# Performance work log

Hardware: AMD Instinct MI355X
Metric: run time of the kernel (lower is better)

Reference implementation:

```python
import jax, jax.numpy as jnp
from jax import lax
import numpy as np

N, D = 1024, 100000
K, SELECT_N = 20, 256  # select_n = int(N * split) = int(1024 * 0.25)


def setup_inputs() -> dict:
    key = jax.random.key(0)
    k1, k2 = jax.random.split(key)
    inp = jax.random.normal(k1, (N, D), dtype=jnp.float32)
    indices = jax.random.randint(k2, (K, SELECT_N), 0, N, dtype=jnp.int32)
    return {"inp": inp, "indices": indices}


def reference(inp, indices):
    # For each of k bagging rounds: gather select_n random rows, max over rows.
    # scan over k keeps the peak intermediate at [select_n, D] instead of [k, select_n, D].
    def step(_, idx):
        return None, jnp.max(inp[idx], axis=0)  # [D]

    _, maxes = lax.scan(step, None, indices)   # [k, D]
    return jnp.mean(maxes, axis=0, keepdims=True)  # [1, D]
```

## Files before the change

kernel.cpp:

```cpp
#include <hip/hip_runtime.h>


#define N_ROWS   1024
#define D_COLS   100000
#define K_ROUNDS 20
#define SEL_N    256
#define NIDX     (K_ROUNDS * SEL_N)
#define CPB      16
#define NBLOCKS  (D_COLS / CPB)
#define BLOCK    256
#define WAVES    4
#define RNDS_PW  (K_ROUNDS / WAVES)
#define NXCD     8
#define NEG_INF  (-3.402823466e+38f)

__global__ __launch_bounds__(BLOCK, 2) void bagmax_kernel(
    const float* __restrict__ inp,
    const int*   __restrict__ indices,
    float*       __restrict__ out)
{
    __shared__ float tile[N_ROWS * CPB];
    __shared__ __align__(16) unsigned short sidx[NIDX];
    __shared__ float wpart[WAVES][CPB];

    const int tid  = threadIdx.x;
    const int lane = tid & 63;
    const int wave = tid >> 6;

    const int orig = blockIdx.x;
    const int q    = NBLOCKS / NXCD;
    const int r8   = NBLOCKS % NXCD;
    const int xcd  = orig & (NXCD - 1);
    const int slot = orig >> 3;
    const int wg   = (xcd < r8 ? xcd * (q + 1) : r8 * (q + 1) + (xcd - r8) * q) + slot;
    const int colbase = wg * CPB;

    for (int i = tid; i < NIDX; i += BLOCK) {
        const int p   = i & 255;
        const int dst = (i & ~255) | ((p & 15) << 4) | (p >> 4);
        sidx[dst] = (unsigned short)indices[i];
    }

    {
        const int ro = tid >> 2;
        const int c4 = (tid & 3) * 4;
        const float* gp = inp + (size_t)ro * D_COLS + colbase + c4;
        #pragma unroll
        for (int it = 0; it < 16; ++it) {
            const int r = it * 64 + ro;
            const float4 v = *reinterpret_cast<const float4*>(gp + (size_t)it * 64 * D_COLS);
            *reinterpret_cast<float4*>(&tile[r * CPB + c4]) = v;
        }
    }
    __syncthreads();

    const int g = lane >> 2;
    const int u = lane & 3;

    float4 rsum = make_float4(0.f, 0.f, 0.f, 0.f);
    #pragma unroll
    for (int kk = 0; kk < RNDS_PW; ++kk) {
        const int k = wave * RNDS_PW + kk;

        const uint4* sp = reinterpret_cast<const uint4*>(&sidx[k * SEL_N + g * 16]);
        const uint4 w0 = sp[0];
        const uint4 w1 = sp[1];
        unsigned int e[16];
        e[0]  = w0.x & 0xFFFFu; e[1]  = w0.x >> 16;
        e[2]  = w0.y & 0xFFFFu; e[3]  = w0.y >> 16;
        e[4]  = w0.z & 0xFFFFu; e[5]  = w0.z >> 16;
        e[6]  = w0.w & 0xFFFFu; e[7]  = w0.w >> 16;
        e[8]  = w1.x & 0xFFFFu; e[9]  = w1.x >> 16;
        e[10] = w1.y & 0xFFFFu; e[11] = w1.y >> 16;
        e[12] = w1.z & 0xFFFFu; e[13] = w1.z >> 16;
        e[14] = w1.w & 0xFFFFu; e[15] = w1.w >> 16;

        float4 a0 = make_float4(NEG_INF, NEG_INF, NEG_INF, NEG_INF);
        float4 a1 = a0;
        #pragma unroll
        for (int i = 0; i < 16; i += 2) {
            const float4 v0 = *reinterpret_cast<const float4*>(&tile[e[i]     * CPB + u * 4]);
            const float4 v1 = *reinterpret_cast<const float4*>(&tile[e[i + 1] * CPB + u * 4]);
            a0.x = fmaxf(a0.x, v0.x); a0.y = fmaxf(a0.y, v0.y);
            a0.z = fmaxf(a0.z, v0.z); a0.w = fmaxf(a0.w, v0.w);
            a1.x = fmaxf(a1.x, v1.x); a1.y = fmaxf(a1.y, v1.y);
            a1.z = fmaxf(a1.z, v1.z); a1.w = fmaxf(a1.w, v1.w);
        }
        float4 acc;
        acc.x = fmaxf(a0.x, a1.x); acc.y = fmaxf(a0.y, a1.y);
        acc.z = fmaxf(a0.z, a1.z); acc.w = fmaxf(a0.w, a1.w);

        #pragma unroll
        for (int s = 4; s <= 32; s <<= 1) {
            acc.x = fmaxf(acc.x, __shfl_xor(acc.x, s, 64));
            acc.y = fmaxf(acc.y, __shfl_xor(acc.y, s, 64));
            acc.z = fmaxf(acc.z, __shfl_xor(acc.z, s, 64));
            acc.w = fmaxf(acc.w, __shfl_xor(acc.w, s, 64));
        }
        rsum.x += acc.x; rsum.y += acc.y; rsum.z += acc.z; rsum.w += acc.w;
    }

    if (g == 0) *reinterpret_cast<float4*>(&wpart[wave][u * 4]) = rsum;
    __syncthreads();

    if (tid < CPB) {
        const float s = wpart[0][tid] + wpart[1][tid] + wpart[2][tid] + wpart[3][tid];
        out[colbase + tid] = s * (1.0f / (float)K_ROUNDS);
    }
}

extern "C" void kernel_launch(void* const* d_in, const int* in_sizes, int n_in,
                              void* d_out, int out_size, void* d_ws, size_t ws_size,
                              hipStream_t stream) {
    const float* inp     = (const float*)d_in[0];
    const int*   indices = (const int*)d_in[1];
    float*       out     = (float*)d_out;

    bagmax_kernel<<<NBLOCKS, BLOCK, 0, stream>>>(inp, indices, out);
}
```

Before: 116.7 us.

## Use persistent blocks with producer/consumer waves and double-buffered LDS tiles

Replaces the one-block-per-16-column-tile launch with a persistent grid of 256 blocks of 512 threads. Four producer waves prefetch the next column tile from global memory into a second LDS buffer while four consumer waves compute the bagged max/mean on the current tile. This hides global load latency behind compute and avoids reloading the index table for every tile. The cost is one block per CU, a __syncthreads per tile, and a grid of only 256 blocks, which may leave CUs underused and reduce memory-level parallelism. The XCD-aware block remapping is also dropped.

```diff
diff --git a/kernel.cpp b/kernel.cpp
--- a/kernel.cpp
+++ b/kernel.cpp
@@ -7,33 +7,25 @@
 #define SEL_N    256
 #define NIDX     (K_ROUNDS * SEL_N)
 #define CPB      16
-#define NBLOCKS  (D_COLS / CPB)
-#define BLOCK    256
-#define WAVES    4
-#define RNDS_PW  (K_ROUNDS / WAVES)
-#define NXCD     8
+#define NT       (D_COLS / CPB)
+#define BLOCK    512
+#define GRID     256
+#define CWAVES   4
+#define RNDS_PW  (K_ROUNDS / CWAVES)
 #define NEG_INF  (-3.402823466e+38f)
 
-__global__ __launch_bounds__(BLOCK, 2) void bagmax_kernel(
+__global__ __launch_bounds__(BLOCK, 1) void bagmax_kernel(
     const float* __restrict__ inp,
     const int*   __restrict__ indices,
     float*       __restrict__ out)
 {
-    __shared__ float tile[N_ROWS * CPB];
+    __shared__ float tile[2][N_ROWS * CPB];
     __shared__ __align__(16) unsigned short sidx[NIDX];
-    __shared__ float wpart[WAVES][CPB];
+    __shared__ float wpart[2][CWAVES][CPB];
 
-    const int tid  = threadIdx.x;
-    const int lane = tid & 63;
-    const int wave = tid >> 6;
-
-    const int orig = blockIdx.x;
-    const int q    = NBLOCKS / NXCD;
-    const int r8   = NBLOCKS % NXCD;
-    const int xcd  = orig & (NXCD - 1);
-    const int slot = orig >> 3;
-    const int wg   = (xcd < r8 ? xcd * (q + 1) : r8 * (q + 1) + (xcd - r8) * q) + slot;
-    const int colbase = wg * CPB;
+    const int tid = threadIdx.x;
+    const int b   = blockIdx.x;
+    const int cnt = (NT - b + GRID - 1) / GRID;
 
     for (int i = tid; i < NIDX; i += BLOCK) {
         const int p   = i & 255;
@@ -42,70 +34,106 @@
     }
 
     {
+        const int colbase = b * CPB;
         const int ro = tid >> 2;
         const int c4 = (tid & 3) * 4;
         const float* gp = inp + (size_t)ro * D_COLS + colbase + c4;
         #pragma unroll
-        for (int it = 0; it < 16; ++it) {
-            const int r = it * 64 + ro;
-            const float4 v = *reinterpret_cast<const float4*>(gp + (size_t)it * 64 * D_COLS);
-            *reinterpret_cast<float4*>(&tile[r * CPB + c4]) = v;
+        for (int it = 0; it < 8; ++it) {
+            const int r = it * 128 + ro;
+            const float4 v = *reinterpret_cast<const float4*>(gp + (size_t)it * 128 * D_COLS);
+            *reinterpret_cast<float4*>(&tile[0][r * CPB + c4]) = v;
         }
     }
     __syncthreads();
 
-    const int g = lane >> 2;
-    const int u = lane & 3;
+    const bool prod = (tid >= 256);
+    const int lane  = tid & 63;
+    const int wave  = (tid >> 6) & 3;
+    const int g     = lane >> 2;
+    const int u     = lane & 3;
 
-    float4 rsum = make_float4(0.f, 0.f, 0.f, 0.f);
-    #pragma unroll
-    for (int kk = 0; kk < RNDS_PW; ++kk) {
-        const int k = wave * RNDS_PW + kk;
+    #pragma unroll 1
+    for (int i = 0; i < cnt; ++i) {
+        const int cur = i & 1;
 
-        const uint4* sp = reinterpret_cast<const uint4*>(&sidx[k * SEL_N + g * 16]);
-        const uint4 w0 = sp[0];
-        const uint4 w1 = sp[1];
-        unsigned int e[16];
-        e[0]  = w0.x & 0xFFFFu; e[1]  = w0.x >> 16;
-        e[2]  = w0.y & 0xFFFFu; e[3]  = w0.y >> 16;
-        e[4]  = w0.z & 0xFFFFu; e[5]  = w0.z >> 16;
-        e[6]  = w0.w & 0xFFFFu; e[7]  = w0.w >> 16;
-        e[8]  = w1.x & 0xFFFFu; e[9]  = w1.x >> 16;
-        e[10] = w1.y & 0xFFFFu; e[11] = w1.y >> 16;
-        e[12] = w1.z & 0xFFFFu; e[13] = w1.z >> 16;
-        e[14] = w1.w & 0xFFFFu; e[15] = w1.w >> 16;
+        if (prod) {
+            if (i + 1 < cnt) {
+                const int ncol = (b + (i + 1) * GRID) * CPB;
+                const int ptid = tid - 256;
+                const int ro = ptid >> 2;
+                const int c4 = (ptid & 3) * 4;
+                const float* gp = inp + (size_t)ro * D_COLS + ncol + c4;
+                float* tb = &tile[cur ^ 1][0];
+                #pragma unroll
+                for (int it = 0; it < 16; ++it) {
+                    const int r = it * 64 + ro;
+                    const float4 v = *reinterpret_cast<const float4*>(gp + (size_t)it * 64 * D_COLS);
+                    *reinterpret_cast<float4*>(&tb[r * CPB + c4]) = v;
+                }
+            }
+        } else {
+            if (i > 0 && tid < CPB) {
+                const int pcol = (b + (i - 1) * GRID) * CPB;
+                const float s = wpart[cur ^ 1][0][tid] + wpart[cur ^ 1][1][tid]
+                              + wpart[cur ^ 1][2][tid] + wpart[cur ^ 1][3][tid];
+                out[pcol + tid] = s * (1.0f / (float)K_ROUNDS);
+            }
 
-        float4 a0 = make_float4(NEG_INF, NEG_INF, NEG_INF, NEG_INF);
-        float4 a1 = a0;
-        #pragma unroll
-        for (int i = 0; i < 16; i += 2) {
-            const float4 v0 = *reinterpret_cast<const float4*>(&tile[e[i]     * CPB + u * 4]);
-            const float4 v1 = *reinterpret_cast<const float4*>(&tile[e[i + 1] * CPB + u * 4]);
-            a0.x = fmaxf(a0.x, v0.x); a0.y = fmaxf(a0.y, v0.y);
-            a0.z = fmaxf(a0.z, v0.z); a0.w = fmaxf(a0.w, v0.w);
-            a1.x = fmaxf(a1.x, v1.x); a1.y = fmaxf(a1.y, v1.y);
-            a1.z = fmaxf(a1.z, v1.z); a1.w = fmaxf(a1.w, v1.w);
+            const float* tb = &tile[cur][0];
+            float4 rsum = make_float4(0.f, 0.f, 0.f, 0.f);
+            #pragma unroll
+            for (int kk = 0; kk < RNDS_PW; ++kk) {
+                const int k = wave * RNDS_PW + kk;
+
+                const uint4* sp = reinterpret_cast<const uint4*>(&sidx[k * SEL_N + g * 16]);
+                const uint4 w0 = sp[0];
+                const uint4 w1 = sp[1];
+                unsigned int e[16];
+                e[0]  = w0.x & 0xFFFFu; e[1]  = w0.x >> 16;
+                e[2]  = w0.y & 0xFFFFu; e[3]  = w0.y >> 16;
+                e[4]  = w0.z & 0xFFFFu; e[5]  = w0.z >> 16;
+                e[6]  = w0.w & 0xFFFFu; e[7]  = w0.w >> 16;
+                e[8]  = w1.x & 0xFFFFu; e[9]  = w1.x >> 16;
+                e[10] = w1.y & 0xFFFFu; e[11] = w1.y >> 16;
+                e[12] = w1.z & 0xFFFFu; e[13] = w1.z >> 16;
+                e[14] = w1.w & 0xFFFFu; e[15] = w1.w >> 16;
+
+                float4 a0 = make_float4(NEG_INF, NEG_INF, NEG_INF, NEG_INF);
+                float4 a1 = a0;
+                #pragma unroll
+                for (int j = 0; j < 16; j += 2) {
+                    const float4 v0 = *reinterpret_cast<const float4*>(&tb[e[j]     * CPB + u * 4]);
+                    const float4 v1 = *reinterpret_cast<const float4*>(&tb[e[j + 1] * CPB + u * 4]);
+                    a0.x = fmaxf(a0.x, v0.x); a0.y = fmaxf(a0.y, v0.y);
+                    a0.z = fmaxf(a0.z, v0.z); a0.w = fmaxf(a0.w, v0.w);
+                    a1.x = fmaxf(a1.x, v1.x); a1.y = fmaxf(a1.y, v1.y);
+                    a1.z = fmaxf(a1.z, v1.z); a1.w = fmaxf(a1.w, v1.w);
+                }
+                float4 acc;
+                acc.x = fmaxf(a0.x, a1.x); acc.y = fmaxf(a0.y, a1.y);
+                acc.z = fmaxf(a0.z, a1.z); acc.w = fmaxf(a0.w, a1.w);
+
+                #pragma unroll
+                for (int s = 4; s <= 32; s <<= 1) {
+                    acc.x = fmaxf(acc.x, __shfl_xor(acc.x, s, 64));
+                    acc.y = fmaxf(acc.y, __shfl_xor(acc.y, s, 64));
+                    acc.z = fmaxf(acc.z, __shfl_xor(acc.z, s, 64));
+                    acc.w = fmaxf(acc.w, __shfl_xor(acc.w, s, 64));
+                }
+                rsum.x += acc.x; rsum.y += acc.y; rsum.z += acc.z; rsum.w += acc.w;
+            }
+            if (g == 0) *reinterpret_cast<float4*>(&wpart[cur][wave][u * 4]) = rsum;
         }
-        float4 acc;
-        acc.x = fmaxf(a0.x, a1.x); acc.y = fmaxf(a0.y, a1.y);
-        acc.z = fmaxf(a0.z, a1.z); acc.w = fmaxf(a0.w, a1.w);
-
-        #pragma unroll
-        for (int s = 4; s <= 32; s <<= 1) {
-            acc.x = fmaxf(acc.x, __shfl_xor(acc.x, s, 64));
-            acc.y = fmaxf(acc.y, __shfl_xor(acc.y, s, 64));
-            acc.z = fmaxf(acc.z, __shfl_xor(acc.z, s, 64));
-            acc.w = fmaxf(acc.w, __shfl_xor(acc.w, s, 64));
-        }
-        rsum.x += acc.x; rsum.y += acc.y; rsum.z += acc.z; rsum.w += acc.w;
+        __syncthreads();
     }
 
-    if (g == 0) *reinterpret_cast<float4*>(&wpart[wave][u * 4]) = rsum;
-    __syncthreads();
-
     if (tid < CPB) {
-        const float s = wpart[0][tid] + wpart[1][tid] + wpart[2][tid] + wpart[3][tid];
-        out[colbase + tid] = s * (1.0f / (float)K_ROUNDS);
+        const int pb   = (cnt - 1) & 1;
+        const int pcol = (b + (cnt - 1) * GRID) * CPB;
+        const float s = wpart[pb][0][tid] + wpart[pb][1][tid]
+                      + wpart[pb][2][tid] + wpart[pb][3][tid];
+        out[pcol + tid] = s * (1.0f / (float)K_ROUNDS);
     }
 }
 
@@ -116,5 +144,5 @@
     const int*   indices = (const int*)d_in[1];
     float*       out     = (float*)d_out;
 
-    bagmax_kernel<<<NBLOCKS, BLOCK, 0, stream>>>(inp, indices, out);
+    bagmax_kernel<<<GRID, BLOCK, 0, stream>>>(inp, indices, out);
 }
```

Measured after the change: 128.3 us. 1.1x slower.

## Use persistent grid with double-buffered LDS tile prefetch and DPP reductions

Applied to the files above, without the earlier changes.

Replaces the one-block-per-16-column launch with a persistent grid of 256 blocks. Each block loops over column tiles and prefetches the next tile into registers while reducing the current one from a double-buffered LDS tile. This amortizes the per-block index staging and launch cost and overlaps global loads with LDS gather work. Part of the cross-lane max reduction now uses DPP row shifts instead of shuffles. The trade-off is lower occupancy (launch bounds 1, doubled LDS, many prefetch registers) and fewer blocks to hide memory latency.

```diff
diff --git a/kernel.cpp b/kernel.cpp
--- a/kernel.cpp
+++ b/kernel.cpp
@@ -7,19 +7,28 @@
 #define SEL_N    256
 #define NIDX     (K_ROUNDS * SEL_N)
 #define CPB      16
-#define NBLOCKS  (D_COLS / CPB)
+#define NT       (D_COLS / CPB)
 #define BLOCK    256
+#define GRID     256
 #define WAVES    4
 #define RNDS_PW  (K_ROUNDS / WAVES)
-#define NXCD     8
 #define NEG_INF  (-3.402823466e+38f)
 
-__global__ __launch_bounds__(BLOCK, 2) void bagmax_kernel(
+template<int CTRL>
+__device__ __forceinline__ float dpp_shr_max(float x) {
+    const int xi = __float_as_int(x);
+    const int sh = __builtin_amdgcn_update_dpp(xi, xi, CTRL, 0xF, 0xF, false);
+    return fmaxf(x, __int_as_float(sh));
+}
+#define ROW_SHR4 0x114
+#define ROW_SHR8 0x118
+
+__global__ __launch_bounds__(BLOCK, 1) void bagmax_kernel(
     const float* __restrict__ inp,
     const int*   __restrict__ indices,
     float*       __restrict__ out)
 {
-    __shared__ float tile[N_ROWS * CPB];
+    __shared__ float tile[2][N_ROWS * CPB];
     __shared__ __align__(16) unsigned short sidx[NIDX];
     __shared__ float wpart[WAVES][CPB];
 
@@ -27,13 +36,9 @@
     const int lane = tid & 63;
     const int wave = tid >> 6;
 
-    const int orig = blockIdx.x;
-    const int q    = NBLOCKS / NXCD;
-    const int r8   = NBLOCKS % NXCD;
-    const int xcd  = orig & (NXCD - 1);
-    const int slot = orig >> 3;
-    const int wg   = (xcd < r8 ? xcd * (q + 1) : r8 * (q + 1) + (xcd - r8) * q) + slot;
-    const int colbase = wg * CPB;
+    const int b   = blockIdx.x;
+    const int swz = (b & 7) * 32 + (b >> 3);
+    const int cnt = (NT - swz + GRID - 1) / GRID;
 
     for (int i = tid; i < NIDX; i += BLOCK) {
         const int p   = i & 255;
@@ -41,71 +46,104 @@
         sidx[dst] = (unsigned short)indices[i];
     }
 
+    const int ro = tid >> 2;
+    const int c4 = (tid & 3) * 4;
+
     {
-        const int ro = tid >> 2;
-        const int c4 = (tid & 3) * 4;
-        const float* gp = inp + (size_t)ro * D_COLS + colbase + c4;
+        const float* gp = inp + (size_t)ro * D_COLS + swz * CPB + c4;
+        float4 v[16];
         #pragma unroll
-        for (int it = 0; it < 16; ++it) {
-            const int r = it * 64 + ro;
-            const float4 v = *reinterpret_cast<const float4*>(gp + (size_t)it * 64 * D_COLS);
-            *reinterpret_cast<float4*>(&tile[r * CPB + c4]) = v;
-        }
+        for (int it = 0; it < 16; ++it)
+            v[it] = *reinterpret_cast<const float4*>(gp + (size_t)it * 64 * D_COLS);
+        #pragma unroll
+        for (int it = 0; it < 16; ++it)
+            *reinterpret_cast<float4*>(&tile[0][(it * 64 + ro) * CPB + c4]) = v[it];
     }
     __syncthreads();
 
     const int g = lane >> 2;
     const int u = lane & 3;
 
-    float4 rsum = make_float4(0.f, 0.f, 0.f, 0.f);
-    #pragma unroll
-    for (int kk = 0; kk < RNDS_PW; ++kk) {
-        const int k = wave * RNDS_PW + kk;
+    #pragma unroll 1
+    for (int i = 0; i < cnt; ++i) {
+        const int cur = i & 1;
+        const bool havenext = (i + 1 < cnt);
 
-        const uint4* sp = reinterpret_cast<const uint4*>(&sidx[k * SEL_N + g * 16]);
-        const uint4 w0 = sp[0];
-        const uint4 w1 = sp[1];
-        unsigned int e[16];
-        e[0]  = w0.x & 0xFFFFu; e[1]  = w0.x >> 16;
-        e[2]  = w0.y & 0xFFFFu; e[3]  = w0.y >> 16;
-        e[4]  = w0.z & 0xFFFFu; e[5]  = w0.z >> 16;
-        e[6]  = w0.w & 0xFFFFu; e[7]  = w0.w >> 16;
-        e[8]  = w1.x & 0xFFFFu; e[9]  = w1.x >> 16;
-        e[10] = w1.y & 0xFFFFu; e[11] = w1.y >> 16;
-        e[12] = w1.z & 0xFFFFu; e[13] = w1.z >> 16;
-        e[14] = w1.w & 0xFFFFu; e[15] = w1.w >> 16;
+        float4 pf[16];
+        if (havenext) {
+            const int ncol = (swz + (i + 1) * GRID) * CPB;
+            const float* gp = inp + (size_t)ro * D_COLS + ncol + c4;
+            #pragma unroll
+            for (int it = 0; it < 16; ++it)
+                pf[it] = *reinterpret_cast<const float4*>(gp + (size_t)it * 64 * D_COLS);
+        }
 
-        float4 a0 = make_float4(NEG_INF, NEG_INF, NEG_INF, NEG_INF);
-        float4 a1 = a0;
+        const float* tb = &tile[cur][0];
+        float4 rsum = make_float4(0.f, 0.f, 0.f, 0.f);
         #pragma unroll
-        for (int i = 0; i < 16; i += 2) {
-            const float4 v0 = *reinterpret_cast<const float4*>(&tile[e[i]     * CPB + u * 4]);
-            const float4 v1 = *reinterpret_cast<const float4*>(&tile[e[i + 1] * CPB + u * 4]);
-            a0.x = fmaxf(a0.x, v0.x); a0.y = fmaxf(a0.y, v0.y);
-            a0.z = fmaxf(a0.z, v0.z); a0.w = fmaxf(a0.w, v0.w);
-            a1.x = fmaxf(a1.x, v1.x); a1.y = fmaxf(a1.y, v1.y);
-            a1.z = fmaxf(a1.z, v1.z); a1.w = fmaxf(a1.w, v1.w);
+        for (int kk = 0; kk < RNDS_PW; ++kk) {
+            const int k = wave * RNDS_PW + kk;
+
+            const uint4* sp = reinterpret_cast<const uint4*>(&sidx[k * SEL_N + g * 16]);
+            const uint4 w0 = sp[0];
+            const uint4 w1 = sp[1];
+            unsigned int e[16];
+            e[0]  = w0.x & 0xFFFFu; e[1]  = w0.x >> 16;
+            e[2]  = w0.y & 0xFFFFu; e[3]  = w0.y >> 16;
+            e[4]  = w0.z & 0xFFFFu; e[5]  = w0.z >> 16;
+            e[6]  = w0.w & 0xFFFFu; e[7]  = w0.w >> 16;
+            e[8]  = w1.x & 0xFFFFu; e[9]  = w1.x >> 16;
+            e[10] = w1.y & 0xFFFFu; e[11] = w1.y >> 16;
+            e[12] = w1.z & 0xFFFFu; e[13] = w1.z >> 16;
+            e[14] = w1.w & 0xFFFFu; e[15] = w1.w >> 16;
+
+            float4 a0 = make_float4(NEG_INF, NEG_INF, NEG_INF, NEG_INF);
+            float4 a1 = a0;
+            #pragma unroll
+            for (int j = 0; j < 16; j += 2) {
+                const float4 v0 = *reinterpret_cast<const float4*>(&tb[e[j]     * CPB + u * 4]);
+                const float4 v1 = *reinterpret_cast<const float4*>(&tb[e[j + 1] * CPB + u * 4]);
+                a0.x = fmaxf(a0.x, v0.x); a0.y = fmaxf(a0.y, v0.y);
+                a0.z = fmaxf(a0.z, v0.z); a0.w = fmaxf(a0.w, v0.w);
+                a1.x = fmaxf(a1.x, v1.x); a1.y = fmaxf(a1.y, v1.y);
+                a1.z = fmaxf(a1.z, v1.z); a1.w = fmaxf(a1.w, v1.w);
+            }
+            float4 acc;
+            acc.x = fmaxf(a0.x, a1.x); acc.y = fmaxf(a0.y, a1.y);
+            acc.z = fmaxf(a0.z, a1.z); acc.w = fmaxf(a0.w, a1.w);
+
+            acc.x = dpp_shr_max<ROW_SHR4>(acc.x); acc.y = dpp_shr_max<ROW_SHR4>(acc.y);
+            acc.z = dpp_shr_max<ROW_SHR4>(acc.z); acc.w = dpp_shr_max<ROW_SHR4>(acc.w);
+            acc.x = dpp_shr_max<ROW_SHR8>(acc.x); acc.y = dpp_shr_max<ROW_SHR8>(acc.y);
+            acc.z = dpp_shr_max<ROW_SHR8>(acc.z); acc.w = dpp_shr_max<ROW_SHR8>(acc.w);
+            acc.x = fmaxf(acc.x, __shfl_xor(acc.x, 16, 64));
+            acc.y = fmaxf(acc.y, __shfl_xor(acc.y, 16, 64));
+            acc.z = fmaxf(acc.z, __shfl_xor(acc.z, 16, 64));
+            acc.w = fmaxf(acc.w, __shfl_xor(acc.w, 16, 64));
+            acc.x = fmaxf(acc.x, __shfl_xor(acc.x, 32, 64));
+            acc.y = fmaxf(acc.y, __shfl_xor(acc.y, 32, 64));
+            acc.z = fmaxf(acc.z, __shfl_xor(acc.z, 32, 64));
+            acc.w = fmaxf(acc.w, __shfl_xor(acc.w, 32, 64));
+
+            rsum.x += acc.x; rsum.y += acc.y; rsum.z += acc.z; rsum.w += acc.w;
         }
-        float4 acc;
-        acc.x = fmaxf(a0.x, a1.x); acc.y = fmaxf(a0.y, a1.y);
-        acc.z = fmaxf(a0.z, a1.z); acc.w = fmaxf(a0.w, a1.w);
+        if (g == 3)
+            *reinterpret_cast<float4*>(&wpart[wave][u * 4]) = rsum;
 
-        #pragma unroll
-        for (int s = 4; s <= 32; s <<= 1) {
-            acc.x = fmaxf(acc.x, __shfl_xor(acc.x, s, 64));
-            acc.y = fmaxf(acc.y, __shfl_xor(acc.y, s, 64));
-            acc.z = fmaxf(acc.z, __shfl_xor(acc.z, s, 64));
-            acc.w = fmaxf(acc.w, __shfl_xor(acc.w, s, 64));
+        __syncthreads();
+
+        if (havenext) {
+            float* tbn = &tile[cur ^ 1][0];
+            #pragma unroll
+            for (int it = 0; it < 16; ++it)
+                *reinterpret_cast<float4*>(&tbn[(it * 64 + ro) * CPB + c4]) = pf[it];
         }
-        rsum.x += acc.x; rsum.y += acc.y; rsum.z += acc.z; rsum.w += acc.w;
-    }
-
-    if (g == 0) *reinterpret_cast<float4*>(&wpart[wave][u * 4]) = rsum;
-    __syncthreads();
-
-    if (tid < CPB) {
-        const float s = wpart[0][tid] + wpart[1][tid] + wpart[2][tid] + wpart[3][tid];
-        out[colbase + tid] = s * (1.0f / (float)K_ROUNDS);
+        if (tid < CPB) {
+            const int col = (swz + i * GRID) * CPB + tid;
+            const float s = wpart[0][tid] + wpart[1][tid] + wpart[2][tid] + wpart[3][tid];
+            out[col] = s * (1.0f / (float)K_ROUNDS);
+        }
+        __syncthreads();
     }
 }
 
@@ -116,5 +154,5 @@
     const int*   indices = (const int*)d_in[1];
     float*       out     = (float*)d_out;
 
-    bagmax_kernel<<<NBLOCKS, BLOCK, 0, stream>>>(inp, indices, out);
+    bagmax_kernel<<<GRID, BLOCK, 0, stream>>>(inp, indices, out);
 }
```

After: 247.6 us. +112.1%, slower.
